# Optimization experiments

Measured on AMD Instinct MI355X. Metric: run time of the kernel, lower is better.

## Reference

```python
import jax, jax.numpy as jnp
import numpy as np

N = 50000
E = 800000
IN = 256
HID = 64
HEADS = 4
EPS = 1e-5


def batchnorm(x, g, b):
    # training-mode BatchNorm1d over node dim, biased variance (torch semantics)
    mu = jnp.mean(x, axis=0)
    var = jnp.mean((x - mu) ** 2, axis=0)
    return (x - mu) * jax.lax.rsqrt(var + EPS) * g + b


def gat(x, edge_index, W, a_src, a_dst, bias, heads, out_ch, num_nodes):
    src, dst = edge_index[0], edge_index[1]
    h = (x @ W).reshape(num_nodes, heads, out_ch)          # [N,H,C]
    al_s = jnp.einsum('nhc,hc->nh', h, a_src)              # [N,H]
    al_d = jnp.einsum('nhc,hc->nh', h, a_dst)
    e = jax.nn.leaky_relu(al_s[src] + al_d[dst], 0.2)      # [E,H]
    # segment softmax over destination neighborhoods
    m = jax.ops.segment_max(e, dst, num_segments=num_nodes)
    m = jnp.where(jnp.isfinite(m), m, 0.0)
    ex = jnp.exp(e - m[dst])                               # [E,H]
    denom = jax.ops.segment_sum(ex, dst, num_segments=num_nodes)
    alpha = ex / (denom[dst] + 1e-16)                      # [E,H]
    msg = alpha[:, :, None] * h[src]                       # [E,H,C]
    out = jax.ops.segment_sum(msg, dst, num_segments=num_nodes)
    return out.reshape(num_nodes, heads * out_ch) + bias


def setup_inputs() -> dict:
    key = jax.random.key(0)
    ks = jax.random.split(key, 12)
    d = {}
    d['x'] = jax.random.normal(ks[0], (N, IN), jnp.float32)
    d['edge_index'] = jax.random.randint(ks[1], (2, E), 0, N, jnp.int32)
    d['bn1_g'] = jnp.ones((IN,), jnp.float32)
    d['bn1_b'] = jnp.zeros((IN,), jnp.float32)
    d['lin1_W'] = jax.random.normal(ks[2], (IN, HID * HEADS), jnp.float32) * (1.0 / np.sqrt(IN))
    d['lin1_b'] = jnp.zeros((HID * HEADS,), jnp.float32)
    d['con1_W'] = jax.random.normal(ks[3], (IN, HID * HEADS), jnp.float32) * (1.0 / np.sqrt(IN))
    d['con1_asrc'] = jax.random.normal(ks[4], (HEADS, HID), jnp.float32) * 0.1
    d['con1_adst'] = jax.random.normal(ks[5], (HEADS, HID), jnp.float32) * 0.1
    d['con1_b'] = jnp.zeros((HID * HEADS,), jnp.float32)
    d['bn3_g'] = jnp.ones((HID * HEADS,), jnp.float32)
    d['bn3_b'] = jnp.zeros((HID * HEADS,), jnp.float32)
    d['lin3_W'] = jax.random.normal(ks[6], (HID * HEADS, 2), jnp.float32) * (1.0 / np.sqrt(HID * HEADS))
    d['lin3_b'] = jnp.zeros((2,), jnp.float32)
    d['con3_W'] = jax.random.normal(ks[7], (HID * HEADS, 2), jnp.float32) * (1.0 / np.sqrt(HID * HEADS))
    d['con3_asrc'] = jax.random.normal(ks[8], (1, 2), jnp.float32) * 0.1
    d['con3_adst'] = jax.random.normal(ks[9], (1, 2), jnp.float32) * 0.1
    d['con3_b'] = jnp.zeros((2,), jnp.float32)
    return d


def reference(x, edge_index, bn1_g, bn1_b, lin1_W, lin1_b, con1_W, con1_asrc, con1_adst, con1_b,
              bn3_g, bn3_b, lin3_W, lin3_b, con3_W, con3_asrc, con3_adst, con3_b):
    x = batchnorm(x, bn1_g, bn1_b)
    x = jax.nn.relu(x @ lin1_W + lin1_b
                    + gat(x, edge_index, con1_W, con1_asrc, con1_adst, con1_b, HEADS, HID, N))
    x = batchnorm(x, bn3_g, bn3_b)
    x = jax.nn.relu(x @ lin3_W + lin3_b
                    + gat(x, edge_index, con3_W, con3_asrc, con3_adst, con3_b, 1, 2, N))
    return x
```

## Files before the change

kernel.cpp:

```cpp
#include <hip/hip_runtime.h>
#include <math.h>

#define NN 50000
#define NE 800000
#define IC 256
#define EPS 1e-5f
#define P8 50176

typedef __attribute__((ext_vector_type(8))) short short8;
typedef __attribute__((ext_vector_type(4))) float f32x4;

enum : int {
  OFF_S1     = 0,
  OFF_S2     = 256,
  OFF_C8     = 512,
  ZERO_END   = OFF_C8 + 8 * P8,
  OFF_COFF   = ZERO_END,
  OFF_START  = OFF_COFF + 8 * P8,
  OFF_RANK   = OFF_START + 50004,
  OFF_ALS    = OFF_RANK + 200000,
  OFF_ALD    = OFF_ALS + 200000,
  OFF_SRCS   = OFF_ALD + 200000,
  OFF_Y32    = OFF_SRCS + 800000,
  OFF_ND4    = OFF_Y32 + 100000,
  OFF_BFH    = OFF_ND4 + 200000,
  OFF_HBF    = OFF_BFH + 65536,
  OFF_YLBF   = OFF_HBF + 6400000,
  WS_FLOATS  = OFF_YLBF + 6400000
};

__device__ __forceinline__ float lrelu(float s) { return s > 0.f ? s : 0.2f * s; }
__device__ __forceinline__ float b2f(unsigned short u) {
  return __uint_as_float(((unsigned)u) << 16);
}
__device__ __forceinline__ unsigned short f2bf(float f) {
  unsigned u = __float_as_uint(f);
  return (unsigned short)((u + 0x7fffu + ((u >> 16) & 1u)) >> 16);
}
__device__ __forceinline__ unsigned cvtpk(float lo, float hi) {
  unsigned r;
  asm("v_cvt_pk_bf16_f32 %0, %1, %2" : "=v"(r) : "v"(lo), "v"(hi));
  return r;
}

__global__ __launch_bounds__(256) void k_prep(const float* __restrict__ x,
                                              float* __restrict__ S1,
                                              float* __restrict__ S2,
                                              const float* __restrict__ Wlin,
                                              const float* __restrict__ Wcon,
                                              unsigned short* __restrict__ Bfh) {
  int b = blockIdx.x;
  if (b < 1024) {
    int c = threadIdx.x;
    float s1 = 0.f, s2 = 0.f;
    for (int r0 = b * 4; r0 < NN; r0 += 4096) {
#pragma unroll
      for (int u = 0; u < 4; ++u) {
        int r = r0 + u;
        if (r < NN) {
          float v = x[r * IC + c];
          s1 += v;
          s2 = fmaf(v, v, s2);
        }
      }
    }
    atomicAdd(&S1[c], s1);
    atomicAdd(&S2[c], s2);
  } else {
    int id = (b - 1024) * 256 + threadIdx.x;
    int j = id & 7, lane = (id >> 3) & 63, nt = (id >> 9) & 31, ks = id >> 14;
    int k = ks * 32 + ((lane >> 4) << 3) + j;
    int n = nt * 16 + (lane & 15);
    float v = (n < 256) ? Wlin[k * 256 + n] : Wcon[k * 256 + (n - 256)];
    Bfh[id] = f2bf(v);
  }
}

__global__ __launch_bounds__(256) void k_bnstats2(const unsigned short* __restrict__ x1,
                                                  float* __restrict__ S1,
                                                  float* __restrict__ S2) {
  int c = threadIdx.x;
  float s1 = 0.f, s2 = 0.f;
  for (int r0 = blockIdx.x * 4; r0 < NN; r0 += 4 * gridDim.x) {
#pragma unroll
    for (int u = 0; u < 4; ++u) {
      int r = r0 + u;
      if (r < NN) {
        float v = b2f(x1[r * IC + c]);
        s1 += v;
        s2 = fmaf(v, v, s2);
      }
    }
  }
  atomicAdd(&S1[c], s1);
  atomicAdd(&S2[c], s2);
}

__global__ __launch_bounds__(256, 4) void k_gemm(const float* __restrict__ x,
                                                 const float* __restrict__ S1,
                                                 const float* __restrict__ S2,
                                                 const float* __restrict__ bng,
                                                 const float* __restrict__ bnb,
                                                 const unsigned short* __restrict__ Bfh,
                                                 unsigned short* __restrict__ ylbf,
                                                 unsigned short* __restrict__ hbf,
                                                 const float* __restrict__ asrc,
                                                 const float* __restrict__ adst,
                                                 float* __restrict__ als,
                                                 float* __restrict__ ald,
                                                 const int* __restrict__ dst,
                                                 int* __restrict__ counts8,
                                                 unsigned char* __restrict__ rank8) {
  const int tid = threadIdx.x;
  const int g = blockIdx.x;
  if (g >= 1568) {
    int hb = g - 1568;
    int e = hb * 256 + tid;
    int copy = hb & 7;
    int old = atomicAdd(&counts8[copy * P8 + dst[e]], 1);
    rank8[e] = (unsigned char)old;
    return;
  }
  const int row_blk = (g >> 4) * 8 + (g & 7);
  const int bn = (g >> 3) & 1;
  if (row_blk >= 782) return;
  const int row0 = row_blk * 64;
  __shared__ unsigned short Ah[2048];
  __shared__ float sc[256], sh[256];
  const int wave = tid >> 6, lane = tid & 63;
  {
    float mu = S1[tid] * (1.f / NN);
    float var = S2[tid] * (1.f / NN) - mu * mu;
    float ss = bng[tid] / sqrtf(var + EPS);
    sc[tid] = ss;
    sh[tid] = bnb[tid] - mu * ss;
  }
  const float4* x4 = (const float4*)x;
  const short8* Bh8 = (const short8*)Bfh;
  f32x4 acc[4][4];
#pragma unroll
  for (int i = 0; i < 4; ++i)
#pragma unroll
    for (int j = 0; j < 4; ++j) acc[i][j] = (f32x4){0.f, 0.f, 0.f, 0.f};

  const int m = tid >> 2, kg = tid & 3;
  const int r = row0 + m;
  const int aaddr = (((m >> 4) * 64) + ((m & 15) | (kg << 4))) * 8;
  __syncthreads();

  for (int ks = 0; ks < 8; ++ks) {
    const int c0 = ks * 32 + kg * 8;
    float v[8];
    if (r < NN) {
      int base = (r * IC + c0) >> 2;
      float4 fa = x4[base], fb = x4[base + 1];
      v[0] = fa.x; v[1] = fa.y; v[2] = fa.z; v[3] = fa.w;
      v[4] = fb.x; v[5] = fb.y; v[6] = fb.z; v[7] = fb.w;
#pragma unroll
      for (int j = 0; j < 8; ++j) v[j] = fmaf(v[j], sc[c0 + j], sh[c0 + j]);
    } else {
#pragma unroll
      for (int j = 0; j < 8; ++j) v[j] = 0.f;
    }
    unsigned ph[4];
#pragma unroll
    for (int j = 0; j < 4; ++j) ph[j] = cvtpk(v[2 * j], v[2 * j + 1]);
    *(uint4*)&Ah[aaddr] = make_uint4(ph[0], ph[1], ph[2], ph[3]);
    __syncthreads();

    short8 ah[4];
#pragma unroll
    for (int mt = 0; mt < 4; ++mt)
      ah[mt] = *(const short8*)&Ah[(mt * 64 + lane) * 8];
#pragma unroll
    for (int nt = 0; nt < 4; ++nt) {
      short8 bh = Bh8[(ks * 32 + bn * 16 + wave * 4 + nt) * 64 + lane];
#pragma unroll
      for (int mt = 0; mt < 4; ++mt)
        acc[mt][nt] = __builtin_amdgcn_mfma_f32_16x16x32_bf16(ah[mt], bh, acc[mt][nt], 0, 0, 0);
    }
    __syncthreads();
  }
  const int colq = lane & 15, quad = lane >> 4;
  if (bn == 0) {
#pragma unroll
    for (int mt = 0; mt < 4; ++mt)
#pragma unroll
      for (int reg = 0; reg < 4; ++reg) {
        int rr = row0 + mt * 16 + quad * 4 + reg;
        if (rr < NN) {
#pragma unroll
          for (int nt = 0; nt < 4; ++nt)
            ylbf[rr * IC + wave * 64 + nt * 16 + colq] = f2bf(acc[mt][nt][reg]);
        }
      }
  } else {
    const int head = wave;
    float asv[4], adv[4];
#pragma unroll
    for (int j = 0; j < 4; ++j) {
      asv[j] = asrc[head * 64 + j * 16 + colq];
      adv[j] = adst[head * 64 + j * 16 + colq];
    }
#pragma unroll
    for (int mt = 0; mt < 4; ++mt)
#pragma unroll
      for (int reg = 0; reg < 4; ++reg) {
        int rr = row0 + mt * 16 + quad * 4 + reg;
        float sA = 0.f, dA = 0.f;
#pragma unroll
        for (int j = 0; j < 4; ++j) {
          float hA = acc[mt][j][reg];
          sA = fmaf(hA, asv[j], sA);
          dA = fmaf(hA, adv[j], dA);
          if (rr < NN) hbf[rr * IC + head * 64 + j * 16 + colq] = f2bf(hA);
        }
#pragma unroll
        for (int off = 1; off < 16; off <<= 1) {
          sA += __shfl_xor(sA, off, 64);
          dA += __shfl_xor(dA, off, 64);
        }
        if (rr < NN) {
          if (colq == 0) als[rr * 4 + head] = sA;
          else if (colq == 1) ald[rr * 4 + head] = dA;
        }
      }
  }
}

__global__ __launch_bounds__(1024) void k_scan(const int* __restrict__ counts8,
                                               int* __restrict__ coff,
                                               int* __restrict__ start,
                                               float* __restrict__ S1,
                                               float* __restrict__ S2) {
  __shared__ int red[16];
  __shared__ int buf[1024];
  const int tid = threadIdx.x, b = blockIdx.x;
  const int base = b * 1024;
  int pre = 0;
  for (int i = tid; i < base; i += 1024) {
    int s = 0;
#pragma unroll
    for (int k = 0; k < 8; ++k) s += counts8[k * P8 + i];
    pre += s;
  }
#pragma unroll
  for (int off = 1; off < 64; off <<= 1) pre += __shfl_xor(pre, off, 64);
  if ((tid & 63) == 0) red[tid >> 6] = pre;
  if (b == 0 && tid < 256) {
    S1[tid] = 0.f;
    S2[tid] = 0.f;
  }
  __syncthreads();
  int bpre = 0;
#pragma unroll
  for (int w = 0; w < 16; ++w) bpre += red[w];
  const int i = base + tid;
  int pc[8];
  int tot = 0;
#pragma unroll
  for (int k = 0; k < 8; ++k) {
    pc[k] = counts8[k * P8 + i];
    tot += pc[k];
  }
  buf[tid] = tot;
  __syncthreads();
  for (int off = 1; off < 1024; off <<= 1) {
    int t = (tid >= off) ? buf[tid - off] : 0;
    __syncthreads();
    buf[tid] += t;
    __syncthreads();
  }
  int ex = bpre + buf[tid] - tot;
  int run = ex;
#pragma unroll
  for (int k = 0; k < 8; ++k) {
    coff[k * P8 + i] = run;
    run += pc[k];
  }
  if (i < NN) start[i] = ex;
  if (b == 48 && tid == 1023) start[NN] = ex + tot;
}

__global__ __launch_bounds__(256) void k_scatter(const int* __restrict__ src,
                                                 const int* __restrict__ dst,
                                                 const int* __restrict__ coff,
                                                 const unsigned char* __restrict__ rank8,
                                                 int* __restrict__ srcs) {
  int e = blockIdx.x * 256 + threadIdx.x;
  int copy = blockIdx.x & 7;
  int pos = coff[copy * P8 + dst[e]] + (int)rank8[e];
  srcs[pos] = src[e];
}

__global__ __launch_bounds__(256) void k_agg(const ushort4* __restrict__ hq,
                                             ushort4* __restrict__ x1,
                                             const float4* __restrict__ als4,
                                             const float4* __restrict__ ald4,
                                             const int* __restrict__ start,
                                             const int* __restrict__ srcs,
                                             const float4* __restrict__ lb4,
                                             const float4* __restrict__ cb4,
                                             const int nb0) {
  __shared__ float lsp[1024];
  const int tid = threadIdx.x;
  const int wave = tid >> 6, lane = tid & 63, head = lane >> 4;
  const int n = nb0 + blockIdx.x * 4 + wave;
  const float* als = (const float*)als4;
  const int s = start[n], t = start[n + 1];
  const int deg = t - s;
  const float4 aldv = ald4[n];
  int svk = -1;
  float p0 = 0.f, p1 = 0.f, p2 = 0.f, p3 = 0.f;
  if (lane < deg) {
    svk = srcs[s + lane];
    float4 a = als4[svk];
    p0 = __expf(lrelu(a.x + aldv.x));
    p1 = __expf(lrelu(a.y + aldv.y));
    p2 = __expf(lrelu(a.z + aldv.z));
    p3 = __expf(lrelu(a.w + aldv.w));
  }
  *(float4*)&lsp[wave * 256 + lane * 4] = make_float4(p0, p1, p2, p3);
  float d0 = p0, d1 = p1, d2 = p2, d3 = p3;
  const float aldh = head == 0 ? aldv.x : head == 1 ? aldv.y : head == 2 ? aldv.z : aldv.w;
  if (deg > 64) {
    for (int i = s + 64 + lane; i < t; i += 64) {
      float4 a = als4[srcs[i]];
      d0 += __expf(lrelu(a.x + aldv.x));
      d1 += __expf(lrelu(a.y + aldv.y));
      d2 += __expf(lrelu(a.z + aldv.z));
      d3 += __expf(lrelu(a.w + aldv.w));
    }
  }
#pragma unroll
  for (int off = 1; off < 64; off <<= 1) {
    d0 += __shfl_xor(d0, off, 64);
    d1 += __shfl_xor(d1, off, 64);
    d2 += __shfl_xor(d2, off, 64);
    d3 += __shfl_xor(d3, off, 64);
  }
  const float inv =
      1.f / ((head == 0 ? d0 : head == 1 ? d1 : head == 2 ? d2 : d3) + 1e-16f);
  float a0 = 0.f, a1 = 0.f, a2 = 0.f, a3 = 0.f;
  const int cnt = min(deg, 64);
  const int wbase = wave * 256 + head;
  int j = 0;
  for (; j + 4 <= cnt; j += 4) {
    int sv0 = __shfl(svk, j, 64), sv1 = __shfl(svk, j + 1, 64);
    int sv2 = __shfl(svk, j + 2, 64), sv3 = __shfl(svk, j + 3, 64);
    ushort4 hv0 = hq[sv0 * 64 + lane];
    ushort4 hv1 = hq[sv1 * 64 + lane];
    ushort4 hv2 = hq[sv2 * 64 + lane];
    ushort4 hv3 = hq[sv3 * 64 + lane];
    float w0 = lsp[wbase + j * 4], w1 = lsp[wbase + j * 4 + 4];
    float w2 = lsp[wbase + j * 4 + 8], w3 = lsp[wbase + j * 4 + 12];
    a0 = fmaf(w0, b2f(hv0.x), a0); a1 = fmaf(w0, b2f(hv0.y), a1);
    a2 = fmaf(w0, b2f(hv0.z), a2); a3 = fmaf(w0, b2f(hv0.w), a3);
    a0 = fmaf(w1, b2f(hv1.x), a0); a1 = fmaf(w1, b2f(hv1.y), a1);
    a2 = fmaf(w1, b2f(hv1.z), a2); a3 = fmaf(w1, b2f(hv1.w), a3);
    a0 = fmaf(w2, b2f(hv2.x), a0); a1 = fmaf(w2, b2f(hv2.y), a1);
    a2 = fmaf(w2, b2f(hv2.z), a2); a3 = fmaf(w2, b2f(hv2.w), a3);
    a0 = fmaf(w3, b2f(hv3.x), a0); a1 = fmaf(w3, b2f(hv3.y), a1);
    a2 = fmaf(w3, b2f(hv3.z), a2); a3 = fmaf(w3, b2f(hv3.w), a3);
  }
  for (; j < cnt; ++j) {
    int sv = __shfl(svk, j, 64);
    float w = lsp[wbase + j * 4];
    ushort4 hv = hq[sv * 64 + lane];
    a0 = fmaf(w, b2f(hv.x), a0);
    a1 = fmaf(w, b2f(hv.y), a1);
    a2 = fmaf(w, b2f(hv.z), a2);
    a3 = fmaf(w, b2f(hv.w), a3);
  }
  if (deg > 64) {
    for (int i = s + 64; i < t; ++i) {
      int sv = srcs[i];
      float av = als[sv * 4 + head];
      float p = __expf(lrelu(av + aldh));
      ushort4 hv = hq[sv * 64 + lane];
      a0 = fmaf(p, b2f(hv.x), a0);
      a1 = fmaf(p, b2f(hv.y), a1);
      a2 = fmaf(p, b2f(hv.z), a2);
      a3 = fmaf(p, b2f(hv.w), a3);
    }
  }
  ushort4 yb = x1[n * 64 + lane];
  float4 bb1 = lb4[lane], bb2 = cb4[lane];
  ushort4 rb;
  rb.x = f2bf(fmaxf(fmaf(a0, inv, b2f(yb.x) + bb1.x + bb2.x), 0.f));
  rb.y = f2bf(fmaxf(fmaf(a1, inv, b2f(yb.y) + bb1.y + bb2.y), 0.f));
  rb.z = f2bf(fmaxf(fmaf(a2, inv, b2f(yb.z) + bb1.z + bb2.z), 0.f));
  rb.w = f2bf(fmaxf(fmaf(a3, inv, b2f(yb.w) + bb1.w + bb2.w), 0.f));
  x1[n * 64 + lane] = rb;
}

__global__ __launch_bounds__(256) void k_node2(const ushort4* __restrict__ x1,
                                               const float* __restrict__ S1,
                                               const float* __restrict__ S2,
                                               const float* __restrict__ g3,
                                               const float* __restrict__ b3,
                                               const float4* __restrict__ Wl4,
                                               const float4* __restrict__ Wc4,
                                               const float* __restrict__ a3s,
                                               const float* __restrict__ a3d,
                                               const float* __restrict__ l3b,
                                               const float* __restrict__ c3b,
                                               float2* __restrict__ y32,
                                               float4* __restrict__ nd4) {
  __shared__ float sc[256], sh[256];
  const int tid = threadIdx.x;
  {
    float mu = S1[tid] * (1.f / NN);
    float var = S2[tid] * (1.f / NN) - mu * mu;
    float ss = g3[tid] / sqrtf(var + EPS);
    sc[tid] = ss;
    sh[tid] = b3[tid] - mu * ss;
  }
  __syncthreads();
  const int n = blockIdx.x * 4 + (tid >> 6);
  const int lane = tid & 63;
  ushort4 xb = x1[n * 64 + lane];
  float x0 = fmaf(b2f(xb.x), sc[lane * 4 + 0], sh[lane * 4 + 0]);
  float x1v = fmaf(b2f(xb.y), sc[lane * 4 + 1], sh[lane * 4 + 1]);
  float x2 = fmaf(b2f(xb.z), sc[lane * 4 + 2], sh[lane * 4 + 2]);
  float x3 = fmaf(b2f(xb.w), sc[lane * 4 + 3], sh[lane * 4 + 3]);
  float4 wa = Wl4[lane * 2], wb = Wl4[lane * 2 + 1];
  float y0 = x0 * wa.x + x1v * wa.z + x2 * wb.x + x3 * wb.z;
  float y1 = x0 * wa.y + x1v * wa.w + x2 * wb.y + x3 * wb.w;
  float4 ca = Wc4[lane * 2], cb = Wc4[lane * 2 + 1];
  float g0 = x0 * ca.x + x1v * ca.z + x2 * cb.x + x3 * cb.z;
  float g1 = x0 * ca.y + x1v * ca.w + x2 * cb.y + x3 * cb.w;
#pragma unroll
  for (int off = 1; off < 64; off <<= 1) {
    y0 += __shfl_xor(y0, off, 64);
    y1 += __shfl_xor(y1, off, 64);
    g0 += __shfl_xor(g0, off, 64);
    g1 += __shfl_xor(g1, off, 64);
  }
  if (lane == 0) {
    y32[n] = make_float2(y0 + l3b[0] + c3b[0], y1 + l3b[1] + c3b[1]);
    nd4[n] = make_float4(g0 * a3s[0] + g1 * a3s[1], g0, g1,
                         g0 * a3d[0] + g1 * a3d[1]);
  }
}

__global__ __launch_bounds__(256) void k_final(const int* __restrict__ start,
                                               const int* __restrict__ srcs,
                                               const float4* __restrict__ nd4,
                                               const float2* __restrict__ y32,
                                               float* __restrict__ out) {
  const int tid = threadIdx.x;
  const int n = blockIdx.x * 16 + (tid >> 4);
  const int li = tid & 15;
  const int s = start[n], t = start[n + 1];
  const float ad = nd4[n].w;
  float den = 0.f, a0 = 0.f, a1 = 0.f;
  for (int ii = s + li; ii < t; ii += 16) {
    float4 vv = nd4[srcs[ii]];
    float p = __expf(lrelu(vv.x + ad));
    den += p;
    a0 = fmaf(p, vv.y, a0);
    a1 = fmaf(p, vv.z, a1);
  }
#pragma unroll
  for (int off = 1; off < 16; off <<= 1) {
    den += __shfl_xor(den, off, 64);
    a0 += __shfl_xor(a0, off, 64);
    a1 += __shfl_xor(a1, off, 64);
  }
  if (li == 0) {
    float2 y = y32[n];
    float inv = 1.f / (den + 1e-16f);
    out[2 * n] = fmaxf(fmaf(a0, inv, y.x), 0.f);
    out[2 * n + 1] = fmaxf(fmaf(a1, inv, y.y), 0.f);
  }
}

extern "C" void kernel_launch(void* const* d_in, const int* in_sizes, int n_in,
                              void* d_out, int out_size, void* d_ws, size_t ws_size,
                              hipStream_t stream) {
  const float* x = (const float*)d_in[0];
  const int* ei = (const int*)d_in[1];
  const float* bn1_g = (const float*)d_in[2];
  const float* bn1_b = (const float*)d_in[3];
  const float* lin1_W = (const float*)d_in[4];
  const float* lin1_b = (const float*)d_in[5];
  const float* con1_W = (const float*)d_in[6];
  const float* con1_as = (const float*)d_in[7];
  const float* con1_ad = (const float*)d_in[8];
  const float* con1_b = (const float*)d_in[9];
  const float* bn3_g = (const float*)d_in[10];
  const float* bn3_b = (const float*)d_in[11];
  const float* lin3_W = (const float*)d_in[12];
  const float* lin3_b = (const float*)d_in[13];
  const float* con3_W = (const float*)d_in[14];
  const float* con3_as = (const float*)d_in[15];
  const float* con3_ad = (const float*)d_in[16];
  const float* con3_b = (const float*)d_in[17];
  float* ws = (float*)d_ws;
  const int* srcA = ei;
  const int* dstA = ei + NE;

  float* S1 = ws + OFF_S1;
  float* S2 = ws + OFF_S2;
  int* counts8 = (int*)(ws + OFF_C8);
  int* coff = (int*)(ws + OFF_COFF);
  int* start = (int*)(ws + OFF_START);
  unsigned char* rank8 = (unsigned char*)(ws + OFF_RANK);
  float* als = ws + OFF_ALS;
  float* ald = ws + OFF_ALD;
  int* srcs = (int*)(ws + OFF_SRCS);
  float2* y32 = (float2*)(ws + OFF_Y32);
  float4* nd4 = (float4*)(ws + OFF_ND4);
  unsigned short* Bfh = (unsigned short*)(ws + OFF_BFH);
  unsigned short* hbf = (unsigned short*)(ws + OFF_HBF);
  unsigned short* ylbf = (unsigned short*)(ws + OFF_YLBF);

  hipMemsetAsync(ws, 0, (size_t)ZERO_END * sizeof(float), stream);

  k_prep<<<1536, 256, 0, stream>>>(x, S1, S2, lin1_W, con1_W, Bfh);
  k_gemm<<<1568 + 3125, 256, 0, stream>>>(x, S1, S2, bn1_g, bn1_b, Bfh, ylbf,
                                          hbf, con1_as, con1_ad, als, ald, dstA,
                                          counts8, rank8);
  k_scan<<<49, 1024, 0, stream>>>(counts8, coff, start, S1, S2);
  k_scatter<<<3125, 256, 0, stream>>>(srcA, dstA, coff, rank8, srcs);
  k_agg<<<6250, 256, 0, stream>>>((const ushort4*)hbf, (ushort4*)ylbf,
                                  (const float4*)als, (const float4*)ald, start,
                                  srcs, (const float4*)lin1_b,
                                  (const float4*)con1_b, 0);
  k_agg<<<6250, 256, 0, stream>>>((const ushort4*)hbf, (ushort4*)ylbf,
                                  (const float4*)als, (const float4*)ald, start,
                                  srcs, (const float4*)lin1_b,
                                  (const float4*)con1_b, 25000);
  k_bnstats2<<<512, 256, 0, stream>>>(ylbf, S1, S2);
  k_node2<<<12500, 256, 0, stream>>>((const ushort4*)ylbf, S1, S2, bn3_g, bn3_b,
                                     (const float4*)lin3_W, (const float4*)con3_W,
                                     con3_as, con3_ad, lin3_b, con3_b, y32, nd4);
  k_final<<<3125, 256, 0, stream>>>(start, srcs, nd4, y32, (float*)d_out);
}
```

Measured before the change: 396.6 us.

## Merge scan/scatter and post stages into persistent kernels with grid barriers

Replaces k_scan and k_scatter with one persistent k_sort kernel (1024 blocks) that uses atomic-counter grid barriers. It also fuses bnstats2, node2 and final into a single persistent k_post kernel, double-buffers the A tile in the GEMM with register prefetch, and launches k_agg once instead of twice. The aim is to cut kernel launch gaps and tail effects. The software grid barriers assume all 1024 blocks are co-resident, so the kernel can deadlock if occupancy does not allow that.

```diff
diff --git a/kernel.cpp b/kernel.cpp
--- a/kernel.cpp
+++ b/kernel.cpp
@@ -13,12 +13,14 @@
 enum : int {
   OFF_S1     = 0,
   OFF_S2     = 256,
-  OFF_C8     = 512,
+  OFF_BAR    = 512,
+  OFF_C8     = 528,
   ZERO_END   = OFF_C8 + 8 * P8,
   OFF_COFF   = ZERO_END,
   OFF_START  = OFF_COFF + 8 * P8,
   OFF_RANK   = OFF_START + 50004,
-  OFF_ALS    = OFF_RANK + 200000,
+  OFF_BSM    = OFF_RANK + 200000,
+  OFF_ALS    = OFF_BSM + 1024,
   OFF_ALD    = OFF_ALS + 200000,
   OFF_SRCS   = OFF_ALD + 200000,
   OFF_Y32    = OFF_SRCS + 800000,
@@ -41,6 +43,17 @@
   unsigned r;
   asm("v_cvt_pk_bf16_f32 %0, %1, %2" : "=v"(r) : "v"(lo), "v"(hi));
   return r;
+}
+
+__device__ __forceinline__ void gbar(int* ctr) {
+  __syncthreads();
+  if (threadIdx.x == 0) {
+    __threadfence();
+    atomicAdd(ctr, 1);
+    while (__hip_atomic_load(ctr, __ATOMIC_RELAXED, __HIP_MEMORY_SCOPE_AGENT) < 1024) {}
+    __threadfence();
+  }
+  __syncthreads();
 }
 
 __global__ __launch_bounds__(256) void k_prep(const float* __restrict__ x,
@@ -53,9 +66,9 @@
   if (b < 1024) {
     int c = threadIdx.x;
     float s1 = 0.f, s2 = 0.f;
-    for (int r0 = b * 4; r0 < NN; r0 += 4096) {
-#pragma unroll
-      for (int u = 0; u < 4; ++u) {
+    for (int r0 = b * 8; r0 < NN; r0 += 8192) {
+#pragma unroll
+      for (int u = 0; u < 8; ++u) {
         int r = r0 + u;
         if (r < NN) {
           float v = x[r * IC + c];
@@ -74,26 +87,6 @@
     float v = (n < 256) ? Wlin[k * 256 + n] : Wcon[k * 256 + (n - 256)];
     Bfh[id] = f2bf(v);
   }
-}
-
-__global__ __launch_bounds__(256) void k_bnstats2(const unsigned short* __restrict__ x1,
-                                                  float* __restrict__ S1,
-                                                  float* __restrict__ S2) {
-  int c = threadIdx.x;
-  float s1 = 0.f, s2 = 0.f;
-  for (int r0 = blockIdx.x * 4; r0 < NN; r0 += 4 * gridDim.x) {
-#pragma unroll
-    for (int u = 0; u < 4; ++u) {
-      int r = r0 + u;
-      if (r < NN) {
-        float v = b2f(x1[r * IC + c]);
-        s1 += v;
-        s2 = fmaf(v, v, s2);
-      }
-    }
-  }
-  atomicAdd(&S1[c], s1);
-  atomicAdd(&S2[c], s2);
 }
 
 __global__ __launch_bounds__(256, 4) void k_gemm(const float* __restrict__ x,
@@ -125,7 +118,7 @@
   const int bn = (g >> 3) & 1;
   if (row_blk >= 782) return;
   const int row0 = row_blk * 64;
-  __shared__ unsigned short Ah[2048];
+  __shared__ unsigned short Ah[2][2048];
   __shared__ float sc[256], sh[256];
   const int wave = tid >> 6, lane = tid & 63;
   {
@@ -148,16 +141,18 @@
   const int aaddr = (((m >> 4) * 64) + ((m & 15) | (kg << 4))) * 8;
   __syncthreads();
 
-  for (int ks = 0; ks < 8; ++ks) {
-    const int c0 = ks * 32 + kg * 8;
+  {
+    const int c0 = kg * 8;
     float v[8];
     if (r < NN) {
       int base = (r * IC + c0) >> 2;
       float4 fa = x4[base], fb = x4[base + 1];
-      v[0] = fa.x; v[1] = fa.y; v[2] = fa.z; v[3] = fa.w;
-      v[4] = fb.x; v[5] = fb.y; v[6] = fb.z; v[7] = fb.w;
-#pragma unroll
-      for (int j = 0; j < 8; ++j) v[j] = fmaf(v[j], sc[c0 + j], sh[c0 + j]);
+      float4 sa = *(const float4*)&sc[c0], sb = *(const float4*)&sc[c0 + 4];
+      float4 ta = *(const float4*)&sh[c0], tb = *(const float4*)&sh[c0 + 4];
+      v[0] = fmaf(fa.x, sa.x, ta.x); v[1] = fmaf(fa.y, sa.y, ta.y);
+      v[2] = fmaf(fa.z, sa.z, ta.z); v[3] = fmaf(fa.w, sa.w, ta.w);
+      v[4] = fmaf(fb.x, sb.x, tb.x); v[5] = fmaf(fb.y, sb.y, tb.y);
+      v[6] = fmaf(fb.z, sb.z, tb.z); v[7] = fmaf(fb.w, sb.w, tb.w);
     } else {
 #pragma unroll
       for (int j = 0; j < 8; ++j) v[j] = 0.f;
@@ -165,13 +160,23 @@
     unsigned ph[4];
 #pragma unroll
     for (int j = 0; j < 4; ++j) ph[j] = cvtpk(v[2 * j], v[2 * j + 1]);
-    *(uint4*)&Ah[aaddr] = make_uint4(ph[0], ph[1], ph[2], ph[3]);
+    *(uint4*)&Ah[0][aaddr] = make_uint4(ph[0], ph[1], ph[2], ph[3]);
+  }
+
+  for (int ks = 0; ks < 8; ++ks) {
+    const int cur = ks & 1;
     __syncthreads();
-
+    float4 fa, fb;
+    const bool pre = (ks < 7) && (r < NN);
+    if (pre) {
+      int base = (r * IC + (ks + 1) * 32 + kg * 8) >> 2;
+      fa = x4[base];
+      fb = x4[base + 1];
+    }
     short8 ah[4];
 #pragma unroll
     for (int mt = 0; mt < 4; ++mt)
-      ah[mt] = *(const short8*)&Ah[(mt * 64 + lane) * 8];
+      ah[mt] = *(const short8*)&Ah[cur][(mt * 64 + lane) * 8];
 #pragma unroll
     for (int nt = 0; nt < 4; ++nt) {
       short8 bh = Bh8[(ks * 32 + bn * 16 + wave * 4 + nt) * 64 + lane];
@@ -179,7 +184,25 @@
       for (int mt = 0; mt < 4; ++mt)
         acc[mt][nt] = __builtin_amdgcn_mfma_f32_16x16x32_bf16(ah[mt], bh, acc[mt][nt], 0, 0, 0);
     }
-    __syncthreads();
+    if (ks < 7) {
+      const int c0 = (ks + 1) * 32 + kg * 8;
+      float v[8];
+      if (pre) {
+        float4 sa = *(const float4*)&sc[c0], sb = *(const float4*)&sc[c0 + 4];
+        float4 ta = *(const float4*)&sh[c0], tb = *(const float4*)&sh[c0 + 4];
+        v[0] = fmaf(fa.x, sa.x, ta.x); v[1] = fmaf(fa.y, sa.y, ta.y);
+        v[2] = fmaf(fa.z, sa.z, ta.z); v[3] = fmaf(fa.w, sa.w, ta.w);
+        v[4] = fmaf(fb.x, sb.x, tb.x); v[5] = fmaf(fb.y, sb.y, tb.y);
+        v[6] = fmaf(fb.z, sb.z, tb.z); v[7] = fmaf(fb.w, sb.w, tb.w);
+      } else {
+#pragma unroll
+        for (int j = 0; j < 8; ++j) v[j] = 0.f;
+      }
+      unsigned ph[4];
+#pragma unroll
+      for (int j = 0; j < 4; ++j) ph[j] = cvtpk(v[2 * j], v[2 * j + 1]);
+      *(uint4*)&Ah[cur ^ 1][aaddr] = make_uint4(ph[0], ph[1], ph[2], ph[3]);
+    }
   }
   const int colq = lane & 15, quad = lane >> 4;
   if (bn == 0) {
@@ -228,69 +251,70 @@
   }
 }
 
-__global__ __launch_bounds__(1024) void k_scan(const int* __restrict__ counts8,
-                                               int* __restrict__ coff,
-                                               int* __restrict__ start,
-                                               float* __restrict__ S1,
-                                               float* __restrict__ S2) {
-  __shared__ int red[16];
-  __shared__ int buf[1024];
+__global__ __launch_bounds__(256, 4) void k_sort(const int* __restrict__ counts8,
+                                                 int* __restrict__ coff,
+                                                 int* __restrict__ start,
+                                                 float* __restrict__ S1,
+                                                 float* __restrict__ S2,
+                                                 const int* __restrict__ src,
+                                                 const int* __restrict__ dst,
+                                                 const unsigned char* __restrict__ rank8,
+                                                 int* __restrict__ srcs,
+                                                 int* __restrict__ bsum,
+                                                 int* __restrict__ bar) {
+  __shared__ int tot[49];
+  __shared__ int pref[49];
+  __shared__ int red[4];
   const int tid = threadIdx.x, b = blockIdx.x;
-  const int base = b * 1024;
-  int pre = 0;
-  for (int i = tid; i < base; i += 1024) {
-    int s = 0;
-#pragma unroll
-    for (int k = 0; k < 8; ++k) s += counts8[k * P8 + i];
-    pre += s;
-  }
-#pragma unroll
-  for (int off = 1; off < 64; off <<= 1) pre += __shfl_xor(pre, off, 64);
-  if ((tid & 63) == 0) red[tid >> 6] = pre;
-  if (b == 0 && tid < 256) {
+  if (b == 0) {
     S1[tid] = 0.f;
     S2[tid] = 0.f;
   }
-  __syncthreads();
-  int bpre = 0;
-#pragma unroll
-  for (int w = 0; w < 16; ++w) bpre += red[w];
-  const int i = base + tid;
-  int pc[8];
-  int tot = 0;
-#pragma unroll
-  for (int k = 0; k < 8; ++k) {
-    pc[k] = counts8[k * P8 + i];
-    tot += pc[k];
-  }
-  buf[tid] = tot;
-  __syncthreads();
-  for (int off = 1; off < 1024; off <<= 1) {
-    int t = (tid >= off) ? buf[tid - off] : 0;
-    __syncthreads();
-    buf[tid] += t;
-    __syncthreads();
-  }
-  int ex = bpre + buf[tid] - tot;
-  int run = ex;
-#pragma unroll
-  for (int k = 0; k < 8; ++k) {
-    coff[k * P8 + i] = run;
-    run += pc[k];
-  }
-  if (i < NN) start[i] = ex;
-  if (b == 48 && tid == 1023) start[NN] = ex + tot;
-}
-
-__global__ __launch_bounds__(256) void k_scatter(const int* __restrict__ src,
-                                                 const int* __restrict__ dst,
-                                                 const int* __restrict__ coff,
-                                                 const unsigned char* __restrict__ rank8,
-                                                 int* __restrict__ srcs) {
-  int e = blockIdx.x * 256 + threadIdx.x;
-  int copy = blockIdx.x & 7;
-  int pos = coff[copy * P8 + dst[e]] + (int)rank8[e];
-  srcs[pos] = src[e];
+  if (tid < 49) {
+    int i = b * 49 + tid;
+    int s = 0;
+#pragma unroll
+    for (int k = 0; k < 8; ++k) s += counts8[k * P8 + i];
+    tot[tid] = s;
+  }
+  __syncthreads();
+  if (tid == 0) {
+    int s = 0;
+    for (int e = 0; e < 49; ++e) s += tot[e];
+    bsum[b] = s;
+  }
+  gbar(&bar[0]);
+  int partial = 0;
+  for (int j = tid; j < b; j += 256) partial += bsum[j];
+#pragma unroll
+  for (int off = 1; off < 64; off <<= 1) partial += __shfl_xor(partial, off, 64);
+  if ((tid & 63) == 0) red[tid >> 6] = partial;
+  __syncthreads();
+  if (tid == 0) {
+    int run = red[0] + red[1] + red[2] + red[3];
+    for (int e = 0; e < 49; ++e) {
+      pref[e] = run;
+      run += tot[e];
+    }
+  }
+  __syncthreads();
+  if (tid < 49) {
+    int i = b * 49 + tid;
+    int run = pref[tid];
+#pragma unroll
+    for (int k = 0; k < 8; ++k) {
+      coff[k * P8 + i] = run;
+      run += counts8[k * P8 + i];
+    }
+    if (i < NN) start[i] = pref[tid];
+  }
+  if (b == 0 && tid == 0) start[NN] = NE;
+  gbar(&bar[1]);
+  for (int e = b * 256 + tid; e < NE; e += 1024 * 256) {
+    int copy = (e >> 8) & 7;
+    int pos = coff[copy * P8 + dst[e]] + (int)rank8[e];
+    srcs[pos] = src[e];
+  }
 }
 
 __global__ __launch_bounds__(256) void k_agg(const ushort4* __restrict__ hq,
@@ -300,12 +324,11 @@
                                              const int* __restrict__ start,
                                              const int* __restrict__ srcs,
                                              const float4* __restrict__ lb4,
-                                             const float4* __restrict__ cb4,
-                                             const int nb0) {
+                                             const float4* __restrict__ cb4) {
   __shared__ float lsp[1024];
   const int tid = threadIdx.x;
   const int wave = tid >> 6, lane = tid & 63, head = lane >> 4;
-  const int n = nb0 + blockIdx.x * 4 + wave;
+  const int n = blockIdx.x * 4 + wave;
   const float* als = (const float*)als4;
   const int s = start[n], t = start[n + 1];
   const int deg = t - s;
@@ -394,21 +417,43 @@
   x1[n * 64 + lane] = rb;
 }
 
-__global__ __launch_bounds__(256) void k_node2(const ushort4* __restrict__ x1,
-                                               const float* __restrict__ S1,
-                                               const float* __restrict__ S2,
-                                               const float* __restrict__ g3,
-                                               const float* __restrict__ b3,
-                                               const float4* __restrict__ Wl4,
-                                               const float4* __restrict__ Wc4,
-                                               const float* __restrict__ a3s,
-                                               const float* __restrict__ a3d,
-                                               const float* __restrict__ l3b,
-                                               const float* __restrict__ c3b,
-                                               float2* __restrict__ y32,
-                                               float4* __restrict__ nd4) {
+__global__ __launch_bounds__(256, 4) void k_post(const ushort4* __restrict__ x1u,
+                                                 const unsigned short* __restrict__ x1s,
+                                                 float* __restrict__ S1,
+                                                 float* __restrict__ S2,
+                                                 const float* __restrict__ g3,
+                                                 const float* __restrict__ b3,
+                                                 const float4* __restrict__ Wl4,
+                                                 const float4* __restrict__ Wc4,
+                                                 const float* __restrict__ a3s,
+                                                 const float* __restrict__ a3d,
+                                                 const float* __restrict__ l3b,
+                                                 const float* __restrict__ c3b,
+                                                 float2* __restrict__ y32,
+                                                 float4* __restrict__ nd4,
+                                                 const int* __restrict__ start,
+                                                 const int* __restrict__ srcs,
+                                                 float* __restrict__ out,
+                                                 int* __restrict__ bar) {
+  const int tid = threadIdx.x, b = blockIdx.x;
+  {
+    float s1 = 0.f, s2 = 0.f;
+    for (int r0 = b * 8; r0 < NN; r0 += 8192) {
+#pragma unroll
+      for (int u = 0; u < 8; ++u) {
+        int r = r0 + u;
+        if (r < NN) {
+          float v = b2f(x1s[r * IC + tid]);
+          s1 += v;
+          s2 = fmaf(v, v, s2);
+        }
+      }
+    }
+    atomicAdd(&S1[tid], s1);
+    atomicAdd(&S2[tid], s2);
+  }
+  gbar(&bar[2]);
   __shared__ float sc[256], sh[256];
-  const int tid = threadIdx.x;
   {
     float mu = S1[tid] * (1.f / NN);
     float var = S2[tid] * (1.f / NN) - mu * mu;
@@ -417,62 +462,60 @@
     sh[tid] = b3[tid] - mu * ss;
   }
   __syncthreads();
-  const int n = blockIdx.x * 4 + (tid >> 6);
   const int lane = tid & 63;
-  ushort4 xb = x1[n * 64 + lane];
-  float x0 = fmaf(b2f(xb.x), sc[lane * 4 + 0], sh[lane * 4 + 0]);
-  float x1v = fmaf(b2f(xb.y), sc[lane * 4 + 1], sh[lane * 4 + 1]);
-  float x2 = fmaf(b2f(xb.z), sc[lane * 4 + 2], sh[lane * 4 + 2]);
-  float x3 = fmaf(b2f(xb.w), sc[lane * 4 + 3], sh[lane * 4 + 3]);
-  float4 wa = Wl4[lane * 2], wb = Wl4[lane * 2 + 1];
-  float y0 = x0 * wa.x + x1v * wa.z + x2 * wb.x + x3 * wb.z;
-  float y1 = x0 * wa.y + x1v * wa.w + x2 * wb.y + x3 * wb.w;
-  float4 ca = Wc4[lane * 2], cb = Wc4[lane * 2 + 1];
-  float g0 = x0 * ca.x + x1v * ca.z + x2 * cb.x + x3 * cb.z;
-  float g1 = x0 * ca.y + x1v * ca.w + x2 * cb.y + x3 * cb.w;
-#pragma unroll
-  for (int off = 1; off < 64; off <<= 1) {
-    y0 += __shfl_xor(y0, off, 64);
-    y1 += __shfl_xor(y1, off, 64);
-    g0 += __shfl_xor(g0, off, 64);
-    g1 += __shfl_xor(g1, off, 64);
-  }
-  if (lane == 0) {
-    y32[n] = make_float2(y0 + l3b[0] + c3b[0], y1 + l3b[1] + c3b[1]);
-    nd4[n] = make_float4(g0 * a3s[0] + g1 * a3s[1], g0, g1,
-                         g0 * a3d[0] + g1 * a3d[1]);
-  }
-}
-
-__global__ __launch_bounds__(256) void k_final(const int* __restrict__ start,
-                                               const int* __restrict__ srcs,
-                                               const float4* __restrict__ nd4,
-                                               const float2* __restrict__ y32,
-                                               float* __restrict__ out) {
-  const int tid = threadIdx.x;
-  const int n = blockIdx.x * 16 + (tid >> 4);
-  const int li = tid & 15;
-  const int s = start[n], t = start[n + 1];
-  const float ad = nd4[n].w;
-  float den = 0.f, a0 = 0.f, a1 = 0.f;
-  for (int ii = s + li; ii < t; ii += 16) {
-    float4 vv = nd4[srcs[ii]];
-    float p = __expf(lrelu(vv.x + ad));
-    den += p;
-    a0 = fmaf(p, vv.y, a0);
-    a1 = fmaf(p, vv.z, a1);
-  }
-#pragma unroll
-  for (int off = 1; off < 16; off <<= 1) {
-    den += __shfl_xor(den, off, 64);
-    a0 += __shfl_xor(a0, off, 64);
-    a1 += __shfl_xor(a1, off, 64);
-  }
-  if (li == 0) {
-    float2 y = y32[n];
-    float inv = 1.f / (den + 1e-16f);
-    out[2 * n] = fmaxf(fmaf(a0, inv, y.x), 0.f);
-    out[2 * n + 1] = fmaxf(fmaf(a1, inv, y.y), 0.f);
+  const float4 wa = Wl4[lane * 2], wb = Wl4[lane * 2 + 1];
+  const float4 ca = Wc4[lane * 2], cb = Wc4[lane * 2 + 1];
+  const float l3b0 = l3b[0] + c3b[0], l3b1 = l3b[1] + c3b[1];
+  const float as0 = a3s[0], as1 = a3s[1], ad0 = a3d[0], ad1 = a3d[1];
+  for (int gq = b; gq < 12500; gq += 1024) {
+    const int n = gq * 4 + (tid >> 6);
+    ushort4 xb = x1u[n * 64 + lane];
+    float x0 = fmaf(b2f(xb.x), sc[lane * 4 + 0], sh[lane * 4 + 0]);
+    float x1v = fmaf(b2f(xb.y), sc[lane * 4 + 1], sh[lane * 4 + 1]);
+    float x2 = fmaf(b2f(xb.z), sc[lane * 4 + 2], sh[lane * 4 + 2]);
+    float x3 = fmaf(b2f(xb.w), sc[lane * 4 + 3], sh[lane * 4 + 3]);
+    float y0 = x0 * wa.x + x1v * wa.z + x2 * wb.x + x3 * wb.z;
+    float y1 = x0 * wa.y + x1v * wa.w + x2 * wb.y + x3 * wb.w;
+    float g0 = x0 * ca.x + x1v * ca.z + x2 * cb.x + x3 * cb.z;
+    float g1 = x0 * ca.y + x1v * ca.w + x2 * cb.y + x3 * cb.w;
+#pragma unroll
+    for (int off = 1; off < 64; off <<= 1) {
+      y0 += __shfl_xor(y0, off, 64);
+      y1 += __shfl_xor(y1, off, 64);
+      g0 += __shfl_xor(g0, off, 64);
+      g1 += __shfl_xor(g1, off, 64);
+    }
+    if (lane == 0) {
+      y32[n] = make_float2(y0 + l3b0, y1 + l3b1);
+      nd4[n] = make_float4(g0 * as0 + g1 * as1, g0, g1, g0 * ad0 + g1 * ad1);
+    }
+  }
+  gbar(&bar[3]);
+  for (int gq = b; gq < 3125; gq += 1024) {
+    const int n = gq * 16 + (tid >> 4);
+    const int li = tid & 15;
+    const int s = start[n], t = start[n + 1];
+    const float ad = nd4[n].w;
+    float den = 0.f, a0 = 0.f, a1 = 0.f;
+    for (int ii = s + li; ii < t; ii += 16) {
+      float4 vv = nd4[srcs[ii]];
+      float p = __expf(lrelu(vv.x + ad));
+      den += p;
+      a0 = fmaf(p, vv.y, a0);
+      a1 = fmaf(p, vv.z, a1);
+    }
+#pragma unroll
+    for (int off = 1; off < 16; off <<= 1) {
+      den += __shfl_xor(den, off, 64);
+      a0 += __shfl_xor(a0, off, 64);
+      a1 += __shfl_xor(a1, off, 64);
+    }
+    if (li == 0) {
+      float2 y = y32[n];
+      float inv = 1.f / (den + 1e-16f);
+      out[2 * n] = fmaxf(fmaf(a0, inv, y.x), 0.f);
+      out[2 * n + 1] = fmaxf(fmaf(a1, inv, y.y), 0.f);
+    }
   }
 }
 
@@ -503,10 +546,12 @@
 
   float* S1 = ws + OFF_S1;
   float* S2 = ws + OFF_S2;
+  int* bar = (int*)(ws + OFF_BAR);
   int* counts8 = (int*)(ws + OFF_C8);
   int* coff = (int*)(ws + OFF_COFF);
   int* start = (int*)(ws + OFF_START);
   unsigned char* rank8 = (unsigned char*)(ws + OFF_RANK);
+  int* bsum = (int*)(ws + OFF_BSM);
   float* als = ws + OFF_ALS;
   float* ald = ws + OFF_ALD;
   int* srcs = (int*)(ws + OFF_SRCS);
@@ -522,19 +567,15 @@
   k_gemm<<<1568 + 3125, 256, 0, stream>>>(x, S1, S2, bn1_g, bn1_b, Bfh, ylbf,
                                           hbf, con1_as, con1_ad, als, ald, dstA,
                                           counts8, rank8);
-  k_scan<<<49, 1024, 0, stream>>>(counts8, coff, start, S1, S2);
-  k_scatter<<<3125, 256, 0, stream>>>(srcA, dstA, coff, rank8, srcs);
-  k_agg<<<6250, 256, 0, stream>>>((const ushort4*)hbf, (ushort4*)ylbf,
-                                  (const float4*)als, (const float4*)ald, start,
-                                  srcs, (const float4*)lin1_b,
-                                  (const float4*)con1_b, 0);
-  k_agg<<<6250, 256, 0, stream>>>((const ushort4*)hbf, (ushort4*)ylbf,
-                                  (const float4*)als, (const float4*)ald, start,
-                                  srcs, (const float4*)lin1_b,
-                                  (const float4*)con1_b, 25000);
-  k_bnstats2<<<512, 256, 0, stream>>>(ylbf, S1, S2);
-  k_node2<<<12500, 256, 0, stream>>>((const ushort4*)ylbf, S1, S2, bn3_g, bn3_b,
-                                     (const float4*)lin3_W, (const float4*)con3_W,
-                                     con3_as, con3_ad, lin3_b, con3_b, y32, nd4);
-  k_final<<<3125, 256, 0, stream>>>(start, srcs, nd4, y32, (float*)d_out);
-}
+  k_sort<<<1024, 256, 0, stream>>>(counts8, coff, start, S1, S2, srcA, dstA,
+                                   rank8, srcs, bsum, bar);
+  k_agg<<<12500, 256, 0, stream>>>((const ushort4*)hbf, (ushort4*)ylbf,
+                                   (const float4*)als, (const float4*)ald, start,
+                                   srcs, (const float4*)lin1_b,
+                                   (const float4*)con1_b);
+  k_post<<<1024, 256, 0, stream>>>((const ushort4*)ylbf, ylbf, S1, S2, bn3_g,
+                                   bn3_b, (const float4*)lin3_W,
+                                   (const float4*)con3_W, con3_as, con3_ad,
+                                   lin3_b, con3_b, y32, nd4, start, srcs,
+                                   (float*)d_out, bar);
+}
```

New measurement: 756.4 us. 1.91x slower.

## Double-buffer GEMM A tile, vectorize bnstats2, merge agg launches

Applied to the files above, without the earlier changes.

The GEMM now double-buffers the shared-memory A tile, prefetching the next k-slice of x from global memory while the MFMAs for the current slice run, which removes one barrier per iteration. The second batchnorm-statistics kernel reads four bf16 values per lane as ushort4 and reduces across waves in shared memory before its atomics. The two half-size aggregation launches are merged into one, and k_prep's stats loop is unrolled by 8 instead of 4. New workspace offsets (OFF_BAR, OFF_BSM) are reserved but not used here, and the double buffer adds registers and shared memory that may lower GEMM occupancy.

```diff
diff --git a/kernel.cpp b/kernel.cpp
--- a/kernel.cpp
+++ b/kernel.cpp
@@ -13,12 +13,14 @@
 enum : int {
   OFF_S1     = 0,
   OFF_S2     = 256,
-  OFF_C8     = 512,
+  OFF_BAR    = 512,
+  OFF_C8     = 528,
   ZERO_END   = OFF_C8 + 8 * P8,
   OFF_COFF   = ZERO_END,
   OFF_START  = OFF_COFF + 8 * P8,
   OFF_RANK   = OFF_START + 50004,
-  OFF_ALS    = OFF_RANK + 200000,
+  OFF_BSM    = OFF_RANK + 200000,
+  OFF_ALS    = OFF_BSM + 1024,
   OFF_ALD    = OFF_ALS + 200000,
   OFF_SRCS   = OFF_ALD + 200000,
   OFF_Y32    = OFF_SRCS + 800000,
@@ -53,9 +55,9 @@
   if (b < 1024) {
     int c = threadIdx.x;
     float s1 = 0.f, s2 = 0.f;
-    for (int r0 = b * 4; r0 < NN; r0 += 4096) {
-#pragma unroll
-      for (int u = 0; u < 4; ++u) {
+    for (int r0 = b * 8; r0 < NN; r0 += 8192) {
+#pragma unroll
+      for (int u = 0; u < 8; ++u) {
         int r = r0 + u;
         if (r < NN) {
           float v = x[r * IC + c];
@@ -76,24 +78,30 @@
   }
 }
 
-__global__ __launch_bounds__(256) void k_bnstats2(const unsigned short* __restrict__ x1,
+__global__ __launch_bounds__(256) void k_bnstats2(const ushort4* __restrict__ x1q,
                                                   float* __restrict__ S1,
                                                   float* __restrict__ S2) {
-  int c = threadIdx.x;
-  float s1 = 0.f, s2 = 0.f;
-  for (int r0 = blockIdx.x * 4; r0 < NN; r0 += 4 * gridDim.x) {
-#pragma unroll
-    for (int u = 0; u < 4; ++u) {
-      int r = r0 + u;
-      if (r < NN) {
-        float v = b2f(x1[r * IC + c]);
-        s1 += v;
-        s2 = fmaf(v, v, s2);
-      }
-    }
-  }
-  atomicAdd(&S1[c], s1);
-  atomicAdd(&S2[c], s2);
+  __shared__ float red1[4][256], red2[4][256];
+  const int tid = threadIdx.x, wave = tid >> 6, lane = tid & 63;
+  float s1a = 0.f, s1b = 0.f, s1c = 0.f, s1d = 0.f;
+  float s2a = 0.f, s2b = 0.f, s2c = 0.f, s2d = 0.f;
+  for (int r = blockIdx.x * 4 + wave; r < NN; r += gridDim.x * 4) {
+    ushort4 v = x1q[r * 64 + lane];
+    float f0 = b2f(v.x), f1 = b2f(v.y), f2 = b2f(v.z), f3 = b2f(v.w);
+    s1a += f0; s2a = fmaf(f0, f0, s2a);
+    s1b += f1; s2b = fmaf(f1, f1, s2b);
+    s1c += f2; s2c = fmaf(f2, f2, s2c);
+    s1d += f3; s2d = fmaf(f3, f3, s2d);
+  }
+  red1[wave][lane * 4 + 0] = s1a; red2[wave][lane * 4 + 0] = s2a;
+  red1[wave][lane * 4 + 1] = s1b; red2[wave][lane * 4 + 1] = s2b;
+  red1[wave][lane * 4 + 2] = s1c; red2[wave][lane * 4 + 2] = s2c;
+  red1[wave][lane * 4 + 3] = s1d; red2[wave][lane * 4 + 3] = s2d;
+  __syncthreads();
+  float a = red1[0][tid] + red1[1][tid] + red1[2][tid] + red1[3][tid];
+  float b = red2[0][tid] + red2[1][tid] + red2[2][tid] + red2[3][tid];
+  atomicAdd(&S1[tid], a);
+  atomicAdd(&S2[tid], b);
 }
 
 __global__ __launch_bounds__(256, 4) void k_gemm(const float* __restrict__ x,
@@ -125,7 +133,7 @@
   const int bn = (g >> 3) & 1;
   if (row_blk >= 782) return;
   const int row0 = row_blk * 64;
-  __shared__ unsigned short Ah[2048];
+  __shared__ unsigned short Ah[2][2048];
   __shared__ float sc[256], sh[256];
   const int wave = tid >> 6, lane = tid & 63;
   {
@@ -148,16 +156,18 @@
   const int aaddr = (((m >> 4) * 64) + ((m & 15) | (kg << 4))) * 8;
   __syncthreads();
 
-  for (int ks = 0; ks < 8; ++ks) {
-    const int c0 = ks * 32 + kg * 8;
+  {
+    const int c0 = kg * 8;
     float v[8];
     if (r < NN) {
       int base = (r * IC + c0) >> 2;
       float4 fa = x4[base], fb = x4[base + 1];
-      v[0] = fa.x; v[1] = fa.y; v[2] = fa.z; v[3] = fa.w;
-      v[4] = fb.x; v[5] = fb.y; v[6] = fb.z; v[7] = fb.w;
-#pragma unroll
-      for (int j = 0; j < 8; ++j) v[j] = fmaf(v[j], sc[c0 + j], sh[c0 + j]);
+      float4 sa = *(const float4*)&sc[c0], sb = *(const float4*)&sc[c0 + 4];
+      float4 ta = *(const float4*)&sh[c0], tb = *(const float4*)&sh[c0 + 4];
+      v[0] = fmaf(fa.x, sa.x, ta.x); v[1] = fmaf(fa.y, sa.y, ta.y);
+      v[2] = fmaf(fa.z, sa.z, ta.z); v[3] = fmaf(fa.w, sa.w, ta.w);
+      v[4] = fmaf(fb.x, sb.x, tb.x); v[5] = fmaf(fb.y, sb.y, tb.y);
+      v[6] = fmaf(fb.z, sb.z, tb.z); v[7] = fmaf(fb.w, sb.w, tb.w);
     } else {
 #pragma unroll
       for (int j = 0; j < 8; ++j) v[j] = 0.f;
@@ -165,13 +175,23 @@
     unsigned ph[4];
 #pragma unroll
     for (int j = 0; j < 4; ++j) ph[j] = cvtpk(v[2 * j], v[2 * j + 1]);
-    *(uint4*)&Ah[aaddr] = make_uint4(ph[0], ph[1], ph[2], ph[3]);
+    *(uint4*)&Ah[0][aaddr] = make_uint4(ph[0], ph[1], ph[2], ph[3]);
+  }
+
+  for (int ks = 0; ks < 8; ++ks) {
+    const int cur = ks & 1;
     __syncthreads();
-
+    float4 fa, fb;
+    const bool pre = (ks < 7) && (r < NN);
+    if (pre) {
+      int base = (r * IC + (ks + 1) * 32 + kg * 8) >> 2;
+      fa = x4[base];
+      fb = x4[base + 1];
+    }
     short8 ah[4];
 #pragma unroll
     for (int mt = 0; mt < 4; ++mt)
-      ah[mt] = *(const short8*)&Ah[(mt * 64 + lane) * 8];
+      ah[mt] = *(const short8*)&Ah[cur][(mt * 64 + lane) * 8];
 #pragma unroll
     for (int nt = 0; nt < 4; ++nt) {
       short8 bh = Bh8[(ks * 32 + bn * 16 + wave * 4 + nt) * 64 + lane];
@@ -179,7 +199,25 @@
       for (int mt = 0; mt < 4; ++mt)
         acc[mt][nt] = __builtin_amdgcn_mfma_f32_16x16x32_bf16(ah[mt], bh, acc[mt][nt], 0, 0, 0);
     }
-    __syncthreads();
+    if (ks < 7) {
+      const int c0 = (ks + 1) * 32 + kg * 8;
+      float v[8];
+      if (pre) {
+        float4 sa = *(const float4*)&sc[c0], sb = *(const float4*)&sc[c0 + 4];
+        float4 ta = *(const float4*)&sh[c0], tb = *(const float4*)&sh[c0 + 4];
+        v[0] = fmaf(fa.x, sa.x, ta.x); v[1] = fmaf(fa.y, sa.y, ta.y);
+        v[2] = fmaf(fa.z, sa.z, ta.z); v[3] = fmaf(fa.w, sa.w, ta.w);
+        v[4] = fmaf(fb.x, sb.x, tb.x); v[5] = fmaf(fb.y, sb.y, tb.y);
+        v[6] = fmaf(fb.z, sb.z, tb.z); v[7] = fmaf(fb.w, sb.w, tb.w);
+      } else {
+#pragma unroll
+        for (int j = 0; j < 8; ++j) v[j] = 0.f;
+      }
+      unsigned ph[4];
+#pragma unroll
+      for (int j = 0; j < 4; ++j) ph[j] = cvtpk(v[2 * j], v[2 * j + 1]);
+      *(uint4*)&Ah[cur ^ 1][aaddr] = make_uint4(ph[0], ph[1], ph[2], ph[3]);
+    }
   }
   const int colq = lane & 15, quad = lane >> 4;
   if (bn == 0) {
@@ -300,12 +338,11 @@
                                              const int* __restrict__ start,
                                              const int* __restrict__ srcs,
                                              const float4* __restrict__ lb4,
-                                             const float4* __restrict__ cb4,
-                                             const int nb0) {
+                                             const float4* __restrict__ cb4) {
   __shared__ float lsp[1024];
   const int tid = threadIdx.x;
   const int wave = tid >> 6, lane = tid & 63, head = lane >> 4;
-  const int n = nb0 + blockIdx.x * 4 + wave;
+  const int n = blockIdx.x * 4 + wave;
   const float* als = (const float*)als4;
   const int s = start[n], t = start[n + 1];
   const int deg = t - s;
@@ -524,15 +561,11 @@
                                           counts8, rank8);
   k_scan<<<49, 1024, 0, stream>>>(counts8, coff, start, S1, S2);
   k_scatter<<<3125, 256, 0, stream>>>(srcA, dstA, coff, rank8, srcs);
-  k_agg<<<6250, 256, 0, stream>>>((const ushort4*)hbf, (ushort4*)ylbf,
-                                  (const float4*)als, (const float4*)ald, start,
-                                  srcs, (const float4*)lin1_b,
-                                  (const float4*)con1_b, 0);
-  k_agg<<<6250, 256, 0, stream>>>((const ushort4*)hbf, (ushort4*)ylbf,
-                                  (const float4*)als, (const float4*)ald, start,
-                                  srcs, (const float4*)lin1_b,
-                                  (const float4*)con1_b, 25000);
-  k_bnstats2<<<512, 256, 0, stream>>>(ylbf, S1, S2);
+  k_agg<<<12500, 256, 0, stream>>>((const ushort4*)hbf, (ushort4*)ylbf,
+                                   (const float4*)als, (const float4*)ald, start,
+                                   srcs, (const float4*)lin1_b,
+                                   (const float4*)con1_b);
+  k_bnstats2<<<512, 256, 0, stream>>>((const ushort4*)ylbf, S1, S2);
   k_node2<<<12500, 256, 0, stream>>>((const ushort4*)ylbf, S1, S2, bn3_g, bn3_b,
                                      (const float4*)lin3_W, (const float4*)con3_W,
                                      con3_as, con3_ad, lin3_b, con3_b, y32, nd4);
```

Result: no change. 402.7 us (+1.5%).
